# Optimization experiments

Hardware: AMD Instinct MI355X
Metric: run time of the kernel (lower is better)

The kernel has to match this reference:

```python
import jax, jax.numpy as jnp
import numpy as np

EMBED = 768
GH = 4        # heads per group
GD = 256      # group dim = GH * head_dim
NSTEPS = 3    # n_pde_steps
DT = 0.05
HJ_H = 0.05   # Heimburg-Jackson dispersion coefficient


def _sh(u, k):
    # shift field content along sequence axis (axis=1) by k with zero boundary
    if k == 0:
        return u
    z = jnp.zeros_like(u)
    if k > 0:
        return z.at[:, k:, :].set(u[:, :-k, :])
    return z.at[:, :k, :].set(u[:, -k:, :])


def _d1(u):
    return 0.5 * (_sh(u, -1) - _sh(u, 1))


def _d2(u):
    return _sh(u, -1) - 2.0 * u + _sh(u, 1)


def _d3(u):
    return 0.5 * (_sh(u, -2) - 2.0 * _sh(u, -1) + 2.0 * _sh(u, 1) - _sh(u, 2))


def _d4(u):
    return _sh(u, -2) - 4.0 * _sh(u, -1) + 6.0 * u - 4.0 * _sh(u, 1) + _sh(u, 2)


def _attn(x, qkv_w, qkv_b, ow, ob, nh):
    # standard causal multi-head attention on one head group
    B, T, D = x.shape
    hd = D // nh
    qkv = x @ qkv_w + qkv_b                      # (B,T,3D)
    q, k, v = jnp.split(qkv, 3, axis=-1)
    heads = lambda a: a.reshape(B, T, nh, hd).transpose(0, 2, 1, 3)
    q, k, v = heads(q), heads(k), heads(v)
    s = jnp.einsum('bhqd,bhkd->bhqk', q, k) * (1.0 / np.sqrt(hd))
    causal = jnp.tril(jnp.ones((T, T), dtype=bool))
    s = jnp.where(causal, s, jnp.asarray(-1e9, s.dtype))
    p = jax.nn.softmax(s, axis=-1)
    o = jnp.einsum('bhqk,bhkd->bhqd', p, v).transpose(0, 2, 1, 3).reshape(B, T, D)
    return o @ ow + ob


def _sine_gordon(u):
    # u_tt = u_xx - sin(u), semi-implicit Euler (leapfrog-like)
    w = jnp.zeros_like(u)
    for _ in range(NSTEPS):
        w = w + DT * (_d2(u) - jnp.sin(u))
        u = u + DT * w
    return u


def _kdv(u):
    # u_t = -6 u u_x - u_xxx, explicit Euler
    for _ in range(NSTEPS):
        u = u + DT * (-6.0 * u * _d1(u) - _d3(u))
    return u


def _hj(u):
    # Heimburg-Jackson: u_tt = d_xx((c0^2 + p u + q u^2) u) - h u_xxxx
    # with c0=1, p=-1, q=1
    w = jnp.zeros_like(u)
    for _ in range(NSTEPS):
        f = u - u * u + u * u * u
        w = w + DT * (_d2(f) - HJ_H * _d4(u))
        u = u + DT * w
    return u


def setup_inputs() -> dict:
    key = jax.random.key(0)
    ks = jax.random.split(key, 16)
    s = 0.02
    d, gd = EMBED, GD
    inp = {'x': jax.random.normal(ks[0], (4, 2048, d), dtype=jnp.float32)}
    inp['in_w'] = jax.random.normal(ks[1], (d, d), jnp.float32) * s
    inp['in_b'] = jnp.zeros((d,), jnp.float32)
    for i, n in enumerate(['sg', 'kdv', 'hj']):
        inp[n + '_qkv_w'] = jax.random.normal(ks[2 + 4 * i], (gd, 3 * gd), jnp.float32) * s
        inp[n + '_qkv_b'] = jnp.zeros((3 * gd,), jnp.float32)
        inp[n + '_out_w'] = jax.random.normal(ks[3 + 4 * i], (gd, gd), jnp.float32) * s
        inp[n + '_out_b'] = jnp.zeros((gd,), jnp.float32)
    inp['out_w'] = jax.random.normal(ks[14], (d, d), jnp.float32) * s
    inp['out_b'] = jnp.zeros((d,), jnp.float32)
    return inp


def reference(x, in_w, in_b,
              sg_qkv_w, sg_qkv_b, sg_out_w, sg_out_b,
              kdv_qkv_w, kdv_qkv_b, kdv_out_w, kdv_out_b,
              hj_qkv_w, hj_qkv_b, hj_out_w, hj_out_b,
              out_w, out_b):
    h = x @ in_w + in_b
    xg = jnp.split(h, [GD, 2 * GD], axis=-1)
    sg = _sine_gordon(_attn(xg[0], sg_qkv_w, sg_qkv_b, sg_out_w, sg_out_b, GH))
    kv = _kdv(_attn(xg[1], kdv_qkv_w, kdv_qkv_b, kdv_out_w, kdv_out_b, GH))
    hj = _hj(_attn(xg[2], hj_qkv_w, hj_qkv_b, hj_out_w, hj_out_b, GH))
    out = jnp.concatenate([sg, kv, hj], axis=-1)
    return out @ out_w + out_b
```

## Files before the change

### kernel.cpp

```cpp
#include <hip/hip_runtime.h>
#include <math.h>

#define B_   4
#define T_   2048
#define D_   768
#define M_   8192
#define GD_  256
#define NH_  4
#define HD_  64

typedef short  s16x8 __attribute__((ext_vector_type(8)));
typedef __bf16 bfx8  __attribute__((ext_vector_type(8)));
typedef float  fx4   __attribute__((ext_vector_type(4)));

#define LOG2E 1.44269504088896f
#define QSCALE (0.125f * LOG2E)

__device__ __forceinline__ short f2bf(float f) {
  union { float f; unsigned u; } v; v.f = f;
  unsigned r = v.u + 0x7fffu + ((v.u >> 16) & 1u);
  return (short)(r >> 16);
}

__device__ __forceinline__ unsigned cvt_pk_bf16(float lo, float hi) {
  unsigned r;
  asm("v_cvt_pk_bf16_f32 %0, %1, %2" : "=v"(r) : "v"(lo), "v"(hi));
  return r;
}

__device__ __forceinline__ void gload16(const void* g, void* l) {
  __builtin_amdgcn_global_load_lds(
      (const __attribute__((address_space(1))) unsigned int*)g,
      (__attribute__((address_space(3))) unsigned int*)l, 16, 0, 0);
}

struct PW { const short* p0; const short* p1; const short* p2; };
struct PB { const float* p0; const float* p1; const float* p2; };
__device__ __forceinline__ const short* selw(const PW& s, int z) {
  return z == 0 ? s.p0 : (z == 1 ? s.p1 : s.p2);
}
__device__ __forceinline__ const float* selb(const PB& s, int z) {
  return z == 0 ? s.p0 : (z == 1 ? s.p1 : s.p2);
}

template<int AT, int OBF, int MODE>
__global__ __launch_bounds__(256) void gemm_mfma(
    const void* __restrict__ Avoid, long sA, int lda,
    PW Wp, PB Bp, int K,
    void* __restrict__ C, long sC, int ldc,
    void* __restrict__ xtra)
{
  __shared__ short As[2][128 * 64];
  __shared__ short Bs[2][64 * 64];

  const int z = blockIdx.z;
  const short* Ab16 = (const short*)Avoid + (long)z * sA;
  const float* Ab32 = (const float*)Avoid + (long)z * sA;
  const short* Wb = selw(Wp, z);
  const float* bb = selb(Bp, z);

  const int n0 = blockIdx.x * 64;
  const int m0 = blockIdx.y * 128;
  const int tid = threadIdx.x, lane = tid & 63, w = tid >> 6;
  const int wm = w >> 1, wn = w & 1;
  const int quad = lane >> 4, mr = lane & 15;

  fx4 acc[4][2] = {};

  auto compute = [&](const short* Ab, const short* Bb) {
#pragma unroll
    for (int ks = 0; ks < 2; ++ks) {
      const int cc = ks * 32 + quad * 8;
      const int swz = cc ^ ((mr & 7) * 8);
      bfx8 af[4], bf[2];
#pragma unroll
      for (int i = 0; i < 4; ++i)
        af[i] = *(const bfx8*)&Ab[(wm * 64 + i * 16 + mr) * 64 + swz];
#pragma unroll
      for (int j = 0; j < 2; ++j)
        bf[j] = *(const bfx8*)&Bb[(wn * 32 + j * 16 + mr) * 64 + swz];
#pragma unroll
      for (int i = 0; i < 4; ++i)
#pragma unroll
        for (int j = 0; j < 2; ++j)
          acc[i][j] = __builtin_amdgcn_mfma_f32_16x16x32_bf16(af[i], bf[j], acc[i][j], 0, 0, 0);
    }
  };

  if (AT) {
    const int r0 = tid >> 3;
    const int cs = (tid & 7) * 8;
    const int wswz = cs ^ ((r0 & 7) * 8);
    s16x8 ar[4], br[2];

    auto loadA = [&](int k0) {
#pragma unroll
      for (int gg = 0; gg < 4; ++gg) {
        const float* p = Ab32 + (long)(m0 + r0 + 32 * gg) * lda + k0 + cs;
        float4 f0 = *(const float4*)p;
        float4 f1 = *(const float4*)(p + 4);
        short o[8] = { f2bf(f0.x), f2bf(f0.y), f2bf(f0.z), f2bf(f0.w),
                       f2bf(f1.x), f2bf(f1.y), f2bf(f1.z), f2bf(f1.w) };
        ar[gg] = *(s16x8*)o;
      }
    };
    auto loadB = [&](int k0) {
#pragma unroll
      for (int hh = 0; hh < 2; ++hh)
        br[hh] = *(const s16x8*)(Wb + (long)(n0 + r0 + 32 * hh) * K + k0 + cs);
    };

    loadA(0); loadB(0);
    for (int k0 = 0; k0 < K; k0 += 64) {
#pragma unroll
      for (int gg = 0; gg < 4; ++gg)
        *(s16x8*)&As[0][(r0 + 32 * gg) * 64 + wswz] = ar[gg];
#pragma unroll
      for (int hh = 0; hh < 2; ++hh)
        *(s16x8*)&Bs[0][(r0 + 32 * hh) * 64 + wswz] = br[hh];
      __syncthreads();
      if (k0 + 64 < K) { loadA(k0 + 64); loadB(k0 + 64); }
      compute(&As[0][0], &Bs[0][0]);
      __syncthreads();
    }
  } else {
    const int lrow = lane >> 3, lcol = lane & 7;

    auto stageA = [&](short* dst, int k0) {
#pragma unroll
      for (int i = 0; i < 4; ++i) {
        const int r = i * 32 + w * 8 + lrow;
        const int swz = (lcol * 8) ^ ((r & 7) * 8);
        gload16(Ab16 + (long)(m0 + r) * lda + k0 + swz,
                dst + (i * 32 + w * 8) * 64);
      }
    };
    auto stageB = [&](short* dst, int k0) {
#pragma unroll
      for (int i = 0; i < 2; ++i) {
        const int r = i * 32 + w * 8 + lrow;
        const int swz = (lcol * 8) ^ ((r & 7) * 8);
        gload16(Wb + (long)(n0 + r) * K + k0 + swz,
                dst + (i * 32 + w * 8) * 64);
      }
    };

    stageA(&As[0][0], 0); stageB(&Bs[0][0], 0);
    const int NT = K >> 6;
    for (int t = 0; t < NT; ++t) {
      const int cur = t & 1;
      if (t + 1 < NT) {
        stageA(&As[cur ^ 1][0], (t + 1) * 64);
        stageB(&Bs[cur ^ 1][0], (t + 1) * 64);
        asm volatile("s_waitcnt vmcnt(6)" ::: "memory");
      } else {
        asm volatile("s_waitcnt vmcnt(0)" ::: "memory");
      }
      __builtin_amdgcn_s_barrier();
      compute(&As[cur][0], &Bs[cur][0]);
      __builtin_amdgcn_s_barrier();
    }
  }

  float* Cf = (float*)C + (long)z * sC;
  short* Cs = (short*)C + (long)z * sC;
#pragma unroll
  for (int j = 0; j < 2; ++j) {
    const int col = n0 + wn * 32 + j * 16 + mr;
    const float bvx = bb[col];
#pragma unroll
    for (int i = 0; i < 4; ++i) {
      const int row0 = m0 + wm * 64 + i * 16 + quad * 4;
      if (MODE == 2) {
        const int rb = row0 >> 11, t0 = row0 & 2047;
        fx4 o;
#pragma unroll
        for (int r = 0; r < 4; ++r) o[r] = acc[i][j][r] + bvx;
        *(fx4*)((float*)xtra + (((long)z * B_ + rb) * GD_ + col) * T_ + t0) = o;
      } else if (MODE == 1 && col >= 512) {
        const int h = (col - 512) >> 6, hd = (col - 512) & 63;
        const int rb = row0 >> 11, t0 = row0 & 2047;
        short o4[4];
#pragma unroll
        for (int r = 0; r < 4; ++r) o4[r] = f2bf(acc[i][j][r] + bvx);
        *(short4*)((short*)xtra + ((((long)z * B_ + rb) * NH_ + h) * HD_ + hd) * T_ + t0) =
            *(short4*)o4;
      } else {
        const float sc = (MODE == 1 && col < 256) ? QSCALE : 1.0f;
#pragma unroll
        for (int r = 0; r < 4; ++r) {
          float v = (acc[i][j][r] + bvx) * sc;
          if (OBF) Cs[(long)(row0 + r) * ldc + col] = f2bf(v);
          else     Cf[(long)(row0 + r) * ldc + col] = v;
        }
      }
    }
  }
}

__global__ __launch_bounds__(256) void flash_attn_mfma(
    short* __restrict__ qkv, const short* __restrict__ vtb)
{
  __shared__ short KsL[2][64 * 64];
  __shared__ short VsL[2][80 * 64];
  __shared__ short Ps[128 * 64];

  const int bid = blockIdx.x;
  const int Q = 15 - (bid / 48);
  const int combo = bid % 48;
  const int g = combo % 3, bh = combo / 3;
  const int b = bh >> 2, h = bh & 3;

  short* base = qkv + ((size_t)g * M_ + (size_t)b * T_) * D_;
  short*       Qp = base + h * HD_;
  const short* Kp = base + GD_ + h * HD_;
  const short* Vtp = vtb + ((((size_t)g * B_ + b) * NH_ + h) * HD_) * T_;

  const int tid = threadIdx.x, lane = tid & 63, w = tid >> 6;
  const int quad = lane >> 4, mr = lane & 15;
  const int q0 = Q * 128, wr = w * 32;
  const int qhi = q0 + wr + 31;

  const int lrow = lane >> 3, lcol = lane & 7;
  const int scsw = (lcol * 8) ^ (lrow * 8);

  {
    const short ov = 0x3F80;
    s16x8 one = { ov, ov, ov, ov, ov, ov, ov, ov };
    const int bufi = tid >> 7, ch = tid & 127;
    *(s16x8*)&VsL[bufi][(64 + (ch >> 3)) * 64 + (ch & 7) * 8] = one;
  }

  auto stage = [&](int buf, int kt2) {
    short* kd = &KsL[buf][(w * 8) * 64];
    short* vd = &VsL[buf][(w * 8) * 64];
    const short* kg = Kp + (size_t)(kt2 * 64 + w * 8 + lrow) * D_ + scsw;
    const short* vg = Vtp + (size_t)(w * 8 + lrow) * T_ + kt2 * 64 + scsw;
    gload16(kg, kd);
    gload16(kg + (size_t)32 * D_, kd + 32 * 64);
    gload16(vg, vd);
    gload16(vg + (size_t)32 * T_, vd + 32 * 64);
  };

  bfx8 aq[2][2];
#pragma unroll
  for (int f = 0; f < 2; ++f)
#pragma unroll
    for (int ks = 0; ks < 2; ++ks)
      aq[f][ks] = *(const bfx8*)(Qp + (size_t)(q0 + wr + f * 16 + mr) * D_ +
                                 ks * 32 + quad * 8);

  stage(0, 0);
  __syncthreads();

  fx4 Oa[2][5] = {};

  char* PsB = (char*)&Ps[0];
  const int rot = (mr & 7) << 4;
  const int swzb = (mr & 7) * 8;

  const int ktmax = 2 * Q + 1;
  for (int kt = 0; kt <= ktmax; ++kt) {
    const int cur = kt & 1;
    if (kt < ktmax) {
      stage(cur ^ 1, kt + 1);
      asm volatile("s_waitcnt vmcnt(4)" ::: "memory");
    } else {
      asm volatile("s_waitcnt vmcnt(0)" ::: "memory");
    }
    __builtin_amdgcn_s_barrier();

    if (kt * 64 <= qhi) {
      const short* Kc = &KsL[cur][0];
      const short* Vc = &VsL[cur][0];

      fx4 st[4][2] = {};
#pragma unroll
      for (int ks = 0; ks < 2; ++ks) {
        const int cc = (ks * 32 + quad * 8) ^ swzb;
        bfx8 bk[4];
#pragma unroll
        for (int jj = 0; jj < 4; ++jj)
          bk[jj] = *(const bfx8*)&Kc[(jj * 16 + mr) * 64 + cc];
#pragma unroll
        for (int jj = 0; jj < 4; ++jj)
#pragma unroll
          for (int f = 0; f < 2; ++f)
            st[jj][f] = __builtin_amdgcn_mfma_f32_16x16x32_bf16(bk[jj], aq[f][ks], st[jj][f], 0, 0, 0);
      }

      if (kt >= 2 * Q) {
#pragma unroll
        for (int jj = 0; jj < 4; ++jj)
#pragma unroll
          for (int f = 0; f < 2; ++f) {
            const int qg = q0 + wr + f * 16 + mr;
            const int kvg0 = kt * 64 + jj * 16 + quad * 4;
#pragma unroll
            for (int r = 0; r < 4; ++r)
              if (kvg0 + r > qg) st[jj][f][r] = -1e30f;
          }
      }

#pragma unroll
      for (int f = 0; f < 2; ++f) {
        const int rowb = (wr + f * 16 + mr) << 7;
#pragma unroll
        for (int jj = 0; jj < 4; ++jj) {
          float e0 = exp2f(st[jj][f][0]);
          float e1 = exp2f(st[jj][f][1]);
          float e2 = exp2f(st[jj][f][2]);
          float e3 = exp2f(st[jj][f][3]);
          unsigned pk0 = cvt_pk_bf16(e0, e1);
          unsigned pk1 = cvt_pk_bf16(e2, e3);
          unsigned long long pv = (unsigned long long)pk0 |
                                  ((unsigned long long)pk1 << 32);
          const int kb = (jj * 32 + quad * 8) ^ rot;
          *(unsigned long long*)(PsB + rowb + kb) = pv;
        }
      }

#pragma unroll
      for (int ks = 0; ks < 2; ++ks) {
        const int cc = (ks * 32 + quad * 8) ^ swzb;
        bfx8 ap[2];
#pragma unroll
        for (int f = 0; f < 2; ++f) {
          const int rowb = (wr + f * 16 + mr) << 7;
          const int kb = (ks * 64 + quad * 16) ^ rot;
          ap[f] = *(const bfx8*)(PsB + rowb + kb);
        }
#pragma unroll
        for (int j = 0; j < 5; ++j) {
          bfx8 bv = *(const bfx8*)&Vc[(j * 16 + mr) * 64 + cc];
#pragma unroll
          for (int f = 0; f < 2; ++f)
            Oa[f][j] = __builtin_amdgcn_mfma_f32_16x16x32_bf16(ap[f], bv, Oa[f][j], 0, 0, 0);
        }
      }
    }
    __builtin_amdgcn_s_barrier();
  }

#pragma unroll
  for (int f = 0; f < 2; ++f)
#pragma unroll
    for (int r = 0; r < 4; ++r) {
      const float inv = 1.0f / Oa[f][4][r];
      const int row = q0 + wr + f * 16 + quad * 4 + r;
#pragma unroll
      for (int j = 0; j < 4; ++j)
        Qp[(size_t)row * D_ + j * 16 + mr] = f2bf(Oa[f][j][r] * inv);
    }
}

__device__ __forceinline__ float fhj(float x) { return x - x * x + x * x * x; }

__global__ __launch_bounds__(256) void pde_kernel(
    const float* __restrict__ ut, short* __restrict__ ubt)
{
  __shared__ float halo[3][2][4];

  const int cg = blockIdx.x, b = blockIdx.y, g = blockIdx.z;
  const int tid = threadIdx.x, w = tid >> 6, lane = tid & 63;
  const int c = w >> 1, half = w & 1;
  const int t0 = half * 1024 + lane * 16;
  const float dt = 0.05f;

  const float* src = ut + (((size_t)g * B_ + b) * GD_ + cg * 2 + c) * T_ + t0;

  float uc[20];
#pragma unroll
  for (int q = 0; q < 4; ++q)
    *(fx4*)&uc[2 + q * 4] = *(const fx4*)(src + q * 4);

  {
    float h0 = __shfl_up(uc[16], 1);
    float h1 = __shfl_up(uc[17], 1);
    float h2 = __shfl_down(uc[2], 1);
    float h3 = __shfl_down(uc[3], 1);
    if (half == 0 && lane == 63) { halo[0][c][0] = uc[16]; halo[0][c][1] = uc[17]; }
    if (half == 1 && lane == 0)  { halo[0][c][2] = uc[2];  halo[0][c][3] = uc[3]; }
    __syncthreads();
    uc[0] = h0; uc[1] = h1; uc[18] = h2; uc[19] = h3;
    if (lane == 0) {
      if (half == 1) { uc[0] = halo[0][c][0]; uc[1] = halo[0][c][1]; }
      else           { uc[0] = 0.f;           uc[1] = 0.f; }
    }
    if (lane == 63) {
      if (half == 0) { uc[18] = halo[0][c][2]; uc[19] = halo[0][c][3]; }
      else           { uc[18] = 0.f;           uc[19] = 0.f; }
    }
  }

  float wreg[16];
#pragma unroll
  for (int i = 0; i < 16; ++i) wreg[i] = 0.f;

  for (int step = 0; step < 3; ++step) {
    float nu[16];
#pragma unroll
    for (int tt = 0; tt < 16; ++tt) {
      float um2 = uc[tt], um1 = uc[tt + 1], u = uc[tt + 2];
      float up1 = uc[tt + 3], up2 = uc[tt + 4];
      if (g == 0) {
        float d2 = up1 - 2.f * u + um1;
        wreg[tt] += dt * (d2 - __sinf(u));
        nu[tt] = u + dt * wreg[tt];
      } else if (g == 1) {
        float d1 = 0.5f * (up1 - um1);
        float d3 = 0.5f * (up2 - 2.f * up1 + 2.f * um1 - um2);
        nu[tt] = u + dt * (-6.f * u * d1 - d3);
      } else {
        float d2f = fhj(up1) - 2.f * fhj(u) + fhj(um1);
        float d4  = up2 - 4.f * up1 + 6.f * u - 4.f * um1 + um2;
        wreg[tt] += dt * (d2f - 0.05f * d4);
        nu[tt] = u + dt * wreg[tt];
      }
    }
    if (step < 2) {
      float h0 = __shfl_up(nu[14], 1);
      float h1 = __shfl_up(nu[15], 1);
      float h2 = __shfl_down(nu[0], 1);
      float h3 = __shfl_down(nu[1], 1);
      if (half == 0 && lane == 63) { halo[step + 1][c][0] = nu[14]; halo[step + 1][c][1] = nu[15]; }
      if (half == 1 && lane == 0)  { halo[step + 1][c][2] = nu[0];  halo[step + 1][c][3] = nu[1]; }
      __syncthreads();
      uc[0] = h0; uc[1] = h1; uc[18] = h2; uc[19] = h3;
      if (lane == 0) {
        if (half == 1) { uc[0] = halo[step + 1][c][0]; uc[1] = halo[step + 1][c][1]; }
        else           { uc[0] = 0.f;                  uc[1] = 0.f; }
      }
      if (lane == 63) {
        if (half == 0) { uc[18] = halo[step + 1][c][2]; uc[19] = halo[step + 1][c][3]; }
        else           { uc[18] = 0.f;                  uc[19] = 0.f; }
      }
    }
#pragma unroll
    for (int i = 0; i < 16; ++i) uc[2 + i] = nu[i];
  }

  short o16[16];
#pragma unroll
  for (int i = 0; i < 16; ++i) o16[i] = f2bf(uc[2 + i]);
  short* dst = ubt + (((size_t)g * B_ + b) * GD_ + cg * 2 + c) * T_ + t0;
#pragma unroll
  for (int q = 0; q < 2; ++q)
    *(s16x8*)(dst + q * 8) = *(s16x8*)&o16[q * 8];
}

__global__ __launch_bounds__(256) void transp_kernel(
    const short* __restrict__ ubt, short* __restrict__ ub)
{
  __shared__ short Ls[32][264];

  const int tt = blockIdx.x;
  const int ct = blockIdx.y;
  const int z  = blockIdx.z;
  const int g = z >> 2, b = z & 3;
  const int tid = threadIdx.x;
  const int c0 = ct * 32, t0 = tt * 256;

  const short* src = ubt + (((size_t)g * B_ + b) * GD_ + c0) * T_ + t0;
#pragma unroll
  for (int it = 0; it < 4; ++it) {
    const int row = (tid >> 5) + it * 8;
    const int col = (tid & 31) * 8;
    *(s16x8*)&Ls[row][col] = *(const s16x8*)(src + (size_t)row * T_ + col);
  }
  __syncthreads();

  short* dst = ub + (size_t)b * T_ * D_ + g * GD_ + c0;
  const int cq = tid & 7, tr = tid >> 3;
#pragma unroll
  for (int p = 0; p < 8; ++p) {
    const int tl = p * 32 + tr;
    short o4[4];
#pragma unroll
    for (int i = 0; i < 4; ++i) o4[i] = Ls[cq * 4 + i][tl];
    *(short4*)(dst + (size_t)(t0 + tl) * D_ + cq * 4) = *(short4*)o4;
  }
}

struct PrepArgs {
  const float* w[8]; short* wt[8];
  int K[8], N[8];
  int tend[8];
};

__global__ __launch_bounds__(256) void prep_kernel(PrepArgs pa)
{
  const int bid = blockIdx.x, tid = threadIdx.x;
  __shared__ float Ws[32][33];
  int ti = 0;
#pragma unroll
  for (int i = 0; i < 8; ++i) if (bid >= pa.tend[i]) ti = i + 1;
  const int tloc = bid - (ti ? pa.tend[ti - 1] : 0);
  const int K = pa.K[ti], N = pa.N[ti];
  const int ntx = N >> 5;
  const int k0 = (tloc / ntx) * 32, n0 = (tloc % ntx) * 32;
  const float* W = pa.w[ti];
  short* WT = pa.wt[ti];
  const int tx = tid & 31, ty = tid >> 5;

#pragma unroll
  for (int i = 0; i < 4; ++i)
    Ws[ty + 8 * i][tx] = W[(long)(k0 + ty + 8 * i) * N + n0 + tx];
  __syncthreads();
#pragma unroll
  for (int i = 0; i < 4; ++i) {
    int r = ty + 8 * i;
    WT[(long)(n0 + r) * K + k0 + tx] = f2bf(Ws[tx][r]);
  }
}

extern "C" void kernel_launch(void* const* d_in, const int* in_sizes, int n_in,
                              void* d_out, int out_size, void* d_ws, size_t ws_size,
                              hipStream_t stream)
{
  (void)in_sizes; (void)n_in; (void)out_size; (void)ws_size;

  const float* x         = (const float*)d_in[0];
  const float* in_w      = (const float*)d_in[1];
  const float* in_b      = (const float*)d_in[2];
  const float* sg_qkv_w  = (const float*)d_in[3];
  const float* sg_qkv_b  = (const float*)d_in[4];
  const float* sg_out_w  = (const float*)d_in[5];
  const float* sg_out_b  = (const float*)d_in[6];
  const float* kdv_qkv_w = (const float*)d_in[7];
  const float* kdv_qkv_b = (const float*)d_in[8];
  const float* kdv_out_w = (const float*)d_in[9];
  const float* kdv_out_b = (const float*)d_in[10];
  const float* hj_qkv_w  = (const float*)d_in[11];
  const float* hj_qkv_b  = (const float*)d_in[12];
  const float* hj_out_w  = (const float*)d_in[13];
  const float* hj_out_b  = (const float*)d_in[14];
  const float* out_w     = (const float*)d_in[15];
  const float* out_b     = (const float*)d_in[16];
  float* out = (float*)d_out;

  const size_t MD = (size_t)M_ * D_;
  short* base = (short*)d_ws;
  short* hb   = base + MD;
  float* uf   = (float*)d_ws;
  short* qkvb = base + 2 * MD;
  short* ub16 = qkvb + 3 * MD;
  short* wts  = ub16 + MD;
  short* in_wT  = wts;
  short* qkvT0  = in_wT + 589824;
  short* qkvT1  = qkvT0 + 196608;
  short* qkvT2  = qkvT1 + 196608;
  short* outT0  = qkvT2 + 196608;
  short* outT1  = outT0 + 65536;
  short* outT2  = outT1 + 65536;
  short* out_wT = outT2 + 65536;
  short* vtb    = out_wT + 589824;
  short* ubt    = qkvb;

  dim3 blk(256);

  PrepArgs pa;
  const float* wsrc[8] = { in_w, sg_qkv_w, kdv_qkv_w, hj_qkv_w,
                           sg_out_w, kdv_out_w, hj_out_w, out_w };
  short* wdst[8] = { in_wT, qkvT0, qkvT1, qkvT2, outT0, outT1, outT2, out_wT };
  int Ksz[8] = { 768, 256, 256, 256, 256, 256, 256, 768 };
  int Nsz[8] = { 768, 768, 768, 768, 256, 256, 256, 768 };
  int cum = 0;
  for (int i = 0; i < 8; ++i) {
    pa.w[i] = wsrc[i]; pa.wt[i] = wdst[i]; pa.K[i] = Ksz[i]; pa.N[i] = Nsz[i];
    cum += (Ksz[i] >> 5) * (Nsz[i] >> 5);
    pa.tend[i] = cum;
  }
  prep_kernel<<<dim3((unsigned)cum), blk, 0, stream>>>(pa);

  gemm_mfma<1, 1, 0><<<dim3(12, 64, 1), blk, 0, stream>>>(
      x, 0, D_, PW{in_wT, in_wT, in_wT}, PB{in_b, in_b, in_b}, D_,
      hb, 0, D_, nullptr);

  gemm_mfma<0, 1, 1><<<dim3(12, 64, 3), blk, 0, stream>>>(
      hb, 256, D_,
      PW{qkvT0, qkvT1, qkvT2}, PB{sg_qkv_b, kdv_qkv_b, hj_qkv_b}, GD_,
      qkvb, (long)MD, D_, vtb);

  flash_attn_mfma<<<dim3(768), blk, 0, stream>>>(qkvb, vtb);

  gemm_mfma<0, 0, 2><<<dim3(4, 64, 3), blk, 0, stream>>>(
      qkvb, (long)MD, D_,
      PW{outT0, outT1, outT2}, PB{sg_out_b, kdv_out_b, hj_out_b}, GD_,
      uf, 0, 0, uf);

  pde_kernel<<<dim3(128, 4, 3), blk, 0, stream>>>(uf, ubt);

  transp_kernel<<<dim3(8, 8, 12), blk, 0, stream>>>(ubt, ub16);

  gemm_mfma<0, 0, 0><<<dim3(12, 64, 1), blk, 0, stream>>>(
      ub16, 0, D_, PW{out_wT, out_wT, out_wT}, PB{out_b, out_b, out_b}, D_,
      out, 0, D_, nullptr);
}
```

Before: 285.3 us.

## Widen GEMM tiles to 128x128, remap blocks per XCD, simplify flash staging

The GEMM tile grows from 128x64 to 128x128, with a 4x4 accumulator per wave and the grids halved in x. Block IDs are remapped so that consecutive tiles land on the same XCD, which should improve L2 reuse. The flash attention kernel drops its async double-buffered swizzled LDS staging and instead prefetches K/V into registers and stores them into padded LDS arrays, using full __syncthreads barriers. Larger tiles cut redundant A loads but raise register and LDS use and lower the block count. The simpler flash pipeline may also lose overlap between loads and compute.

```diff
diff --git a/kernel.cpp b/kernel.cpp
--- a/kernel.cpp
+++ b/kernel.cpp
@@ -51,7 +51,7 @@
     void* __restrict__ xtra)
 {
   __shared__ short As[2][128 * 64];
-  __shared__ short Bs[2][64 * 64];
+  __shared__ short Bs[AT ? 1 : 2][128 * 64];
 
   const int z = blockIdx.z;
   const short* Ab16 = (const short*)Avoid + (long)z * sA;
@@ -59,30 +59,36 @@
   const short* Wb = selw(Wp, z);
   const float* bb = selb(Bp, z);
 
-  const int n0 = blockIdx.x * 64;
-  const int m0 = blockIdx.y * 128;
+  const int nx = gridDim.x, nwg = nx * gridDim.y;
+  const int orig = blockIdx.y * nx + blockIdx.x;
+  const int xcd = orig & 7, loc = orig >> 3;
+  const int qq = nwg >> 3, rr = nwg & 7;
+  const int wg = (xcd < rr ? xcd * (qq + 1) : rr * (qq + 1) + (xcd - rr) * qq) + loc;
+  const int n0 = (wg % nx) * 128;
+  const int m0 = (wg / nx) * 128;
+
   const int tid = threadIdx.x, lane = tid & 63, w = tid >> 6;
   const int wm = w >> 1, wn = w & 1;
   const int quad = lane >> 4, mr = lane & 15;
 
-  fx4 acc[4][2] = {};
+  fx4 acc[4][4] = {};
 
   auto compute = [&](const short* Ab, const short* Bb) {
 #pragma unroll
     for (int ks = 0; ks < 2; ++ks) {
       const int cc = ks * 32 + quad * 8;
       const int swz = cc ^ ((mr & 7) * 8);
-      bfx8 af[4], bf[2];
+      bfx8 af[4], bf[4];
 #pragma unroll
       for (int i = 0; i < 4; ++i)
         af[i] = *(const bfx8*)&Ab[(wm * 64 + i * 16 + mr) * 64 + swz];
 #pragma unroll
-      for (int j = 0; j < 2; ++j)
-        bf[j] = *(const bfx8*)&Bb[(wn * 32 + j * 16 + mr) * 64 + swz];
+      for (int j = 0; j < 4; ++j)
+        bf[j] = *(const bfx8*)&Bb[(wn * 64 + j * 16 + mr) * 64 + swz];
 #pragma unroll
       for (int i = 0; i < 4; ++i)
 #pragma unroll
-        for (int j = 0; j < 2; ++j)
+        for (int j = 0; j < 4; ++j)
           acc[i][j] = __builtin_amdgcn_mfma_f32_16x16x32_bf16(af[i], bf[j], acc[i][j], 0, 0, 0);
     }
   };
@@ -91,7 +97,7 @@
     const int r0 = tid >> 3;
     const int cs = (tid & 7) * 8;
     const int wswz = cs ^ ((r0 & 7) * 8);
-    s16x8 ar[4], br[2];
+    s16x8 ar[4], br[4];
 
     auto loadA = [&](int k0) {
 #pragma unroll
@@ -106,7 +112,7 @@
     };
     auto loadB = [&](int k0) {
 #pragma unroll
-      for (int hh = 0; hh < 2; ++hh)
+      for (int hh = 0; hh < 4; ++hh)
         br[hh] = *(const s16x8*)(Wb + (long)(n0 + r0 + 32 * hh) * K + k0 + cs);
     };
 
@@ -116,7 +122,7 @@
       for (int gg = 0; gg < 4; ++gg)
         *(s16x8*)&As[0][(r0 + 32 * gg) * 64 + wswz] = ar[gg];
 #pragma unroll
-      for (int hh = 0; hh < 2; ++hh)
+      for (int hh = 0; hh < 4; ++hh)
         *(s16x8*)&Bs[0][(r0 + 32 * hh) * 64 + wswz] = br[hh];
       __syncthreads();
       if (k0 + 64 < K) { loadA(k0 + 64); loadB(k0 + 64); }
@@ -137,7 +143,7 @@
     };
     auto stageB = [&](short* dst, int k0) {
 #pragma unroll
-      for (int i = 0; i < 2; ++i) {
+      for (int i = 0; i < 4; ++i) {
         const int r = i * 32 + w * 8 + lrow;
         const int swz = (lcol * 8) ^ ((r & 7) * 8);
         gload16(Wb + (long)(n0 + r) * K + k0 + swz,
@@ -152,7 +158,7 @@
       if (t + 1 < NT) {
         stageA(&As[cur ^ 1][0], (t + 1) * 64);
         stageB(&Bs[cur ^ 1][0], (t + 1) * 64);
-        asm volatile("s_waitcnt vmcnt(6)" ::: "memory");
+        asm volatile("s_waitcnt vmcnt(8)" ::: "memory");
       } else {
         asm volatile("s_waitcnt vmcnt(0)" ::: "memory");
       }
@@ -165,8 +171,8 @@
   float* Cf = (float*)C + (long)z * sC;
   short* Cs = (short*)C + (long)z * sC;
 #pragma unroll
-  for (int j = 0; j < 2; ++j) {
-    const int col = n0 + wn * 32 + j * 16 + mr;
+  for (int j = 0; j < 4; ++j) {
+    const int col = n0 + wn * 64 + j * 16 + mr;
     const float bvx = bb[col];
 #pragma unroll
     for (int i = 0; i < 4; ++i) {
@@ -201,8 +207,8 @@
 __global__ __launch_bounds__(256) void flash_attn_mfma(
     short* __restrict__ qkv, const short* __restrict__ vtb)
 {
-  __shared__ short KsL[2][64 * 64];
-  __shared__ short VsL[2][80 * 64];
+  __shared__ short Ks[64][72];
+  __shared__ short Vs[80][72];
   __shared__ short Ps[128 * 64];
 
   const int bid = blockIdx.x;
@@ -221,26 +227,13 @@
   const int q0 = Q * 128, wr = w * 32;
   const int qhi = q0 + wr + 31;
 
-  const int lrow = lane >> 3, lcol = lane & 7;
-  const int scsw = (lcol * 8) ^ (lrow * 8);
-
-  {
+  const int sra = tid >> 3, sc = (tid & 7) * 8;
+
+  if (tid < 128) {
     const short ov = 0x3F80;
     s16x8 one = { ov, ov, ov, ov, ov, ov, ov, ov };
-    const int bufi = tid >> 7, ch = tid & 127;
-    *(s16x8*)&VsL[bufi][(64 + (ch >> 3)) * 64 + (ch & 7) * 8] = one;
-  }
-
-  auto stage = [&](int buf, int kt2) {
-    short* kd = &KsL[buf][(w * 8) * 64];
-    short* vd = &VsL[buf][(w * 8) * 64];
-    const short* kg = Kp + (size_t)(kt2 * 64 + w * 8 + lrow) * D_ + scsw;
-    const short* vg = Vtp + (size_t)(w * 8 + lrow) * T_ + kt2 * 64 + scsw;
-    gload16(kg, kd);
-    gload16(kg + (size_t)32 * D_, kd + 32 * 64);
-    gload16(vg, vd);
-    gload16(vg + (size_t)32 * T_, vd + 32 * 64);
-  };
+    *(s16x8*)&Vs[64 + (tid >> 3)][(tid & 7) * 8] = one;
+  }
 
   bfx8 aq[2][2];
 #pragma unroll
@@ -250,38 +243,40 @@
       aq[f][ks] = *(const bfx8*)(Qp + (size_t)(q0 + wr + f * 16 + mr) * D_ +
                                  ks * 32 + quad * 8);
 
-  stage(0, 0);
-  __syncthreads();
+  s16x8 kreg0 = *(const s16x8*)(Kp + (size_t)sra * D_ + sc);
+  s16x8 kreg1 = *(const s16x8*)(Kp + (size_t)(sra + 32) * D_ + sc);
+  s16x8 vreg0 = *(const s16x8*)(Vtp + (size_t)sra * T_ + sc);
+  s16x8 vreg1 = *(const s16x8*)(Vtp + (size_t)(sra + 32) * T_ + sc);
 
   fx4 Oa[2][5] = {};
 
   char* PsB = (char*)&Ps[0];
   const int rot = (mr & 7) << 4;
-  const int swzb = (mr & 7) * 8;
 
   const int ktmax = 2 * Q + 1;
   for (int kt = 0; kt <= ktmax; ++kt) {
-    const int cur = kt & 1;
+    *(s16x8*)&Ks[sra][sc]      = kreg0;
+    *(s16x8*)&Ks[sra + 32][sc] = kreg1;
+    *(s16x8*)&Vs[sra][sc]      = vreg0;
+    *(s16x8*)&Vs[sra + 32][sc] = vreg1;
+    __syncthreads();
+
     if (kt < ktmax) {
-      stage(cur ^ 1, kt + 1);
-      asm volatile("s_waitcnt vmcnt(4)" ::: "memory");
-    } else {
-      asm volatile("s_waitcnt vmcnt(0)" ::: "memory");
-    }
-    __builtin_amdgcn_s_barrier();
+      const int kn = (kt + 1) * 64;
+      kreg0 = *(const s16x8*)(Kp + (size_t)(kn + sra) * D_ + sc);
+      kreg1 = *(const s16x8*)(Kp + (size_t)(kn + sra + 32) * D_ + sc);
+      vreg0 = *(const s16x8*)(Vtp + (size_t)sra * T_ + kn + sc);
+      vreg1 = *(const s16x8*)(Vtp + (size_t)(sra + 32) * T_ + kn + sc);
+    }
 
     if (kt * 64 <= qhi) {
-      const short* Kc = &KsL[cur][0];
-      const short* Vc = &VsL[cur][0];
-
       fx4 st[4][2] = {};
 #pragma unroll
       for (int ks = 0; ks < 2; ++ks) {
-        const int cc = (ks * 32 + quad * 8) ^ swzb;
         bfx8 bk[4];
 #pragma unroll
         for (int jj = 0; jj < 4; ++jj)
-          bk[jj] = *(const bfx8*)&Kc[(jj * 16 + mr) * 64 + cc];
+          bk[jj] = *(const bfx8*)&Ks[jj * 16 + mr][ks * 32 + quad * 8];
 #pragma unroll
         for (int jj = 0; jj < 4; ++jj)
 #pragma unroll
@@ -322,7 +317,6 @@
 
 #pragma unroll
       for (int ks = 0; ks < 2; ++ks) {
-        const int cc = (ks * 32 + quad * 8) ^ swzb;
         bfx8 ap[2];
 #pragma unroll
         for (int f = 0; f < 2; ++f) {
@@ -332,14 +326,14 @@
         }
 #pragma unroll
         for (int j = 0; j < 5; ++j) {
-          bfx8 bv = *(const bfx8*)&Vc[(j * 16 + mr) * 64 + cc];
+          bfx8 bv = *(const bfx8*)&Vs[j * 16 + mr][ks * 32 + quad * 8];
 #pragma unroll
           for (int f = 0; f < 2; ++f)
             Oa[f][j] = __builtin_amdgcn_mfma_f32_16x16x32_bf16(ap[f], bv, Oa[f][j], 0, 0, 0);
         }
       }
     }
-    __builtin_amdgcn_s_barrier();
+    __syncthreads();
   }
 
 #pragma unroll
@@ -573,18 +567,18 @@
   }
   prep_kernel<<<dim3((unsigned)cum), blk, 0, stream>>>(pa);
 
-  gemm_mfma<1, 1, 0><<<dim3(12, 64, 1), blk, 0, stream>>>(
+  gemm_mfma<1, 1, 0><<<dim3(6, 64, 1), blk, 0, stream>>>(
       x, 0, D_, PW{in_wT, in_wT, in_wT}, PB{in_b, in_b, in_b}, D_,
       hb, 0, D_, nullptr);
 
-  gemm_mfma<0, 1, 1><<<dim3(12, 64, 3), blk, 0, stream>>>(
+  gemm_mfma<0, 1, 1><<<dim3(6, 64, 3), blk, 0, stream>>>(
       hb, 256, D_,
       PW{qkvT0, qkvT1, qkvT2}, PB{sg_qkv_b, kdv_qkv_b, hj_qkv_b}, GD_,
       qkvb, (long)MD, D_, vtb);
 
   flash_attn_mfma<<<dim3(768), blk, 0, stream>>>(qkvb, vtb);
 
-  gemm_mfma<0, 0, 2><<<dim3(4, 64, 3), blk, 0, stream>>>(
+  gemm_mfma<0, 0, 2><<<dim3(2, 64, 3), blk, 0, stream>>>(
       qkvb, (long)MD, D_,
       PW{outT0, outT1, outT2}, PB{sg_out_b, kdv_out_b, hj_out_b}, GD_,
       uf, 0, 0, uf);
@@ -593,7 +587,7 @@
 
   transp_kernel<<<dim3(8, 8, 12), blk, 0, stream>>>(ubt, ub16);
 
-  gemm_mfma<0, 0, 0><<<dim3(12, 64, 1), blk, 0, stream>>>(
+  gemm_mfma<0, 0, 0><<<dim3(6, 64, 1), blk, 0, stream>>>(
       ub16, 0, D_, PW{out_wT, out_wT, out_wT}, PB{out_b, out_b, out_b}, D_,
       out, 0, D_, nullptr);
 }
```

Measured after the change: 267.1 us. 1.07x faster.
